# Kernel optimization log

Hardware: AMD Instinct MI355X
Metric: run time of the kernel (lower is better)

The kernel has to match this reference:

```python
import jax, jax.numpy as jnp
import numpy as np
from math import factorial

PI_A = 3.1415926  # the literal used in the original module
L = 16
NORDER = 5
PERIOD = 200.0


def _lpmv(m, n, x):
    """Associated Legendre P_n^m(x), m>=0, with Condon-Shortley phase (scipy convention)."""
    pmm = np.ones_like(x)
    if m > 0:
        dfact = float(np.prod(np.arange(1, 2 * m, 2, dtype=np.float64)))  # (2m-1)!!
        pmm = ((-1.0) ** m) * dfact * (1.0 - x * x) ** (m / 2.0)
    if n == m:
        return pmm
    pmmp1 = x * (2 * m + 1) * pmm
    if n == m + 1:
        return pmmp1
    for ll in range(m + 2, n + 1):
        pll = ((2 * ll - 1) * x * pmmp1 - (ll + m - 1) * pmm) / (ll - m)
        pmm, pmmp1 = pmmp1, pll
    return pmmp1


def _sh(m, n, ph, th):
    """Real SH matching the original `sh` helper. NOTE: the original uses `-1 ** m`,
    which in Python is -(1**m) == -1 for all m; we reproduce that faithfully."""
    ma = abs(m)
    N = np.sqrt((2 * n + 1) / (4.0 * np.pi) * factorial(n - ma) / factorial(n + ma))
    P = _lpmv(ma, n, np.cos(th))
    if m < 0:
        return (-np.sqrt(2.0) * N * P * np.sin(ma * ph)).astype(np.float32)
    if m == 0:
        return (N * P).astype(np.float32)
    return (-np.sqrt(2.0) * N * P * np.cos(ma * ph)).astype(np.float32)


def _grids():
    th, ph = np.meshgrid(
        (np.arange(L, dtype=np.float64) + 0.5) * PI_A / L,
        (np.arange(2 * L, dtype=np.float64) + 0.5) * PI_A / L,
        indexing='ij',
    )
    return th, ph  # each [L, 2L]


def setup_inputs() -> dict:
    key = jax.random.key(0)
    B = 65536
    lightid = jax.random.randint(key, (B,), 0, 256, dtype=jnp.int32)  # values unused; only size matters
    th, ph = _grids()
    mlist = [x for m in range(NORDER) for x in range(-m, m + 1)]
    nlist = [m for m in range(NORDER) for x in range(-m, m + 1)]
    bases = np.stack([_sh(m, n, ph, th) for m, n in zip(mlist, nlist)], axis=0)  # [25, L, 2L]
    return {"lightid": lightid, "iternum": 1000, "bases": jnp.asarray(bases)}


def reference(lightid, iternum, bases):
    B = lightid.shape[0]
    th_np, ph_np = _grids()
    th = jnp.asarray(th_np, dtype=jnp.float32)   # [L, 2L]
    ph = jnp.asarray(ph_np, dtype=jnp.float32)

    # Rotating light direction, computed in float64 (matches original per-sample python floats)
    ph0 = (iternum * B + np.arange(B, dtype=np.float64)) * 2.0 * PI_A / PERIOD  # [B]
    ldir = jnp.asarray(
        np.stack([np.sin(ph0), np.zeros(B), np.cos(ph0)], axis=-1).astype(np.float32)
    )  # [B, 3]

    # Per-pixel ray directions on the sphere grid
    dr = jnp.stack([jnp.sin(th) * jnp.sin(ph), jnp.cos(th), jnp.sin(th) * jnp.cos(ph)], axis=-1)  # [L, 2L, 3]

    dot = jnp.clip(jnp.einsum('bc,yxc->byx', ldir, dr), -1.0, 1.0)          # [B, L, 2L]
    lm = jnp.log(1e-5 + jnp.exp(-4.0 * jnp.arccos(dot) ** 2))               # gaussian lobe in log space
    lm = lm + 7.0 - jax.nn.logsumexp(lm, axis=(1, 2), keepdims=True)        # normalize total energy

    # SH projection: fold sin(theta) area weight and pi^2/numel into the basis
    numel = L * 2 * L
    w = bases * jnp.sin(th[:, 0])[None, :, None] * (np.pi ** 2 / numel)     # [25, L, 2L]
    proj = jnp.einsum('byx,kyx->bk', lm + 0.001, w)                         # [B, 25]

    return jnp.repeat(proj, 3, axis=1)
```

## Files before the change

### kernel.cpp

```cpp
#include <hip/hip_runtime.h>
#include <math.h>


#define PI_A 3.1415926
#define NPI  3.14159265358979323846

#if __has_builtin(__builtin_amdgcn_sqrtf)
#define FSQRT __builtin_amdgcn_sqrtf
#else
#define FSQRT sqrtf
#endif
#if __has_builtin(__builtin_amdgcn_exp2f)
#define FEXP2 __builtin_amdgcn_exp2f
#else
#define FEXP2 exp2f
#endif
#if __has_builtin(__builtin_amdgcn_logf)
#define FLOG2 __builtin_amdgcn_logf
#else
#define FLOG2 log2f
#endif

#define WT_OFF   0
#define WSUM_OFF 6400
#define TBL_OFF  6432

__global__ __launch_bounds__(256) void sh_prep_kernel(
        const float* __restrict__ bases, float* __restrict__ ws) {
    const int tid = threadIdx.x;
    const int k   = blockIdx.x;
    const float KC = (float)(NPI * NPI / 512.0);

    const int p = tid;
    const int y = p >> 5, x = p & 31;
    const float th_lo = (float)(((double)y + 0.5) * PI_A / 16.0);
    const float th_hi = (float)(((double)(15 - y) + 0.5) * PI_A / 16.0);
    const float v = bases[k * 512 + p] * (sinf(th_lo) * KC)
                  + bases[k * 512 + ((15 - y) << 5) + x] * (sinf(th_hi) * KC);
    ws[WT_OFF + p * 25 + k] = v;

    float s = v;
#pragma unroll
    for (int off = 32; off; off >>= 1) s += __shfl_down(s, off, 64);
    __shared__ float red[4];
    if ((tid & 63) == 0) red[tid >> 6] = s;
    __syncthreads();
    if (tid == 0) ws[WSUM_OFF + k] = red[0] + red[1] + red[2] + red[3];
}

__global__ __launch_bounds__(256) void sh_table_kernel(
        const int* __restrict__ iternum_p, float* __restrict__ ws, int B) {
    __shared__ float lmbuf[8 * 33];
    __shared__ float partial[8][26];
    __shared__ float Sred[4];

    const int tid = threadIdx.x;
    const int j   = blockIdx.x;

    const long long n = (long long)(*iternum_p) * (long long)B + (long long)j;
    const double ph0 = ((double)n * 2.0) * PI_A / 200.0;
    const float sld = (float)sin(ph0);
    const float cld = (float)cos(ph0);

    const int y = tid >> 5, x = tid & 31;
    const float th = (float)(((double)y + 0.5) * PI_A / 16.0);
    const float ph = (float)(((double)x + 0.5) * PI_A / 16.0);
    const float st  = sinf(th);
    const float drx = st * sinf(ph);
    const float drz = st * cosf(ph);
    float dot = fminf(1.0f, fmaxf(-1.0f, sld * drx + cld * drz));
    const float ax = fabsf(dot);
    const float sq = FSQRT(1.0f - ax);
    const float P  = fmaf(fmaf(fmaf(-0.0187293f, ax, 0.0742610f),
                               ax, -0.2121144f), ax, 1.5707288f);
    const float r_ = sq * P;
    const float a  = (dot < 0.0f) ? (3.14159265f - r_) : r_;
    const float c1 = -4.0f * 1.4426950408889634f;
    const float ln2 = 0.6931471805599453f;
    const float ex = FEXP2(a * a * c1);
    const float e  = 1e-5f + ex;
    const float lm = FLOG2(e) * ln2;
    lmbuf[(tid >> 5) * 33 + (tid & 31)] = lm;

    float s = e;
#pragma unroll
    for (int off = 32; off; off >>= 1) s += __shfl_down(s, off, 64);
    if ((tid & 63) == 0) Sred[tid >> 6] = s;
    __syncthreads();

    const int g = tid >> 5, k = tid & 31;
    if (k < 25) {
        float acc = 0.0f;
#pragma unroll
        for (int j2 = 0; j2 < 32; ++j2) {
            acc = fmaf(lmbuf[g * 33 + j2],
                       ws[WT_OFF + (g * 32 + j2) * 25 + k], acc);
        }
        partial[g][k] = acc;
    }
    __syncthreads();

    if (tid < 25) {
        float tot = 0.0f;
#pragma unroll
        for (int gg = 0; gg < 8; ++gg) tot += partial[gg][tid];
        const float S = Sred[0] + Sred[1] + Sred[2] + Sred[3];
        const float C = (7.0f - FLOG2(2.0f * S) * ln2) + 0.001f;
        const float v = tot + C * ws[WSUM_OFF + tid];
        float* tb = ws + TBL_OFF + j * 75 + 3 * tid;
        tb[0] = v; tb[1] = v; tb[2] = v;
    }
}

__global__ __launch_bounds__(256) void sh_bcast_kernel(
        const float* __restrict__ ws, float4* __restrict__ out, int total4) {
    const float4* t4 = (const float4*)(ws + TBL_OFF);
    int i = blockIdx.x * 256 + threadIdx.x;
    const int stride = gridDim.x * 256;
    for (; i < total4; i += stride)
        out[i] = t4[i % 3750];
}

extern "C" void kernel_launch(void* const* d_in, const int* in_sizes, int n_in,
                              void* d_out, int out_size, void* d_ws, size_t ws_size,
                              hipStream_t stream) {
    const int* iternum = (const int*)d_in[1];
    const float* bases = (const float*)d_in[2];
    float* ws = (float*)d_ws;
    const int B = in_sizes[0];
    const int total4 = out_size / 4;

    hipLaunchKernelGGL(sh_prep_kernel, dim3(25), dim3(256), 0, stream, bases, ws);
    hipLaunchKernelGGL(sh_table_kernel, dim3(200), dim3(256), 0, stream,
                       iternum, ws, B);
    int nblk = (total4 + 255) / 256;
    if (nblk > 2048) nblk = 2048;
    hipLaunchKernelGGL(sh_bcast_kernel, dim3(nblk), dim3(256), 0, stream,
                       ws, (float4*)d_out, total4);
}
```

Measured before the change: 18.07 us.

## Fuse prep, table and broadcast kernels into one single-launch kernel

```diff
diff --git a/kernel.cpp b/kernel.cpp
--- a/kernel.cpp
+++ b/kernel.cpp
@@ -4,6 +4,7 @@
 
 #define PI_A 3.1415926
 #define NPI  3.14159265358979323846
+#define SPLIT 4
 
 #if __has_builtin(__builtin_amdgcn_sqrtf)
 #define FSQRT __builtin_amdgcn_sqrtf
@@ -21,51 +22,40 @@
 #define FLOG2 log2f
 #endif
 
-#define WT_OFF   0
-#define WSUM_OFF 6400
-#define TBL_OFF  6432
+__global__ __launch_bounds__(256) void sh_fused_kernel(
+        const int* __restrict__ iternum_p, const float* __restrict__ bases,
+        float* __restrict__ out, int B) {
+    __shared__ float wt[256 * 25];
+    __shared__ float lmbuf[8 * 33];
+    __shared__ float partial[8][26];
+    __shared__ float wpartial[8][26];
+    __shared__ float Sred[4];
+    __shared__ float vrow[76];
 
-__global__ __launch_bounds__(256) void sh_prep_kernel(
-        const float* __restrict__ bases, float* __restrict__ ws) {
     const int tid = threadIdx.x;
-    const int k   = blockIdx.x;
-    const float KC = (float)(NPI * NPI / 512.0);
+    const int j   = blockIdx.x % 200;
+    const int s   = blockIdx.x / 200;
 
-    const int p = tid;
-    const int y = p >> 5, x = p & 31;
+    const float KC  = (float)(NPI * NPI / 512.0);
+    const float ln2 = 0.6931471805599453f;
+
+    const int p = tid, y = p >> 5, x = p & 31;
     const float th_lo = (float)(((double)y + 0.5) * PI_A / 16.0);
     const float th_hi = (float)(((double)(15 - y) + 0.5) * PI_A / 16.0);
-    const float v = bases[k * 512 + p] * (sinf(th_lo) * KC)
-                  + bases[k * 512 + ((15 - y) << 5) + x] * (sinf(th_hi) * KC);
-    ws[WT_OFF + p * 25 + k] = v;
-
-    float s = v;
+    const float st_lo = sinf(th_lo) * KC;
+    const float st_hi = sinf(th_hi) * KC;
+    const int mir = ((15 - y) << 5) + x;
 #pragma unroll
-    for (int off = 32; off; off >>= 1) s += __shfl_down(s, off, 64);
-    __shared__ float red[4];
-    if ((tid & 63) == 0) red[tid >> 6] = s;
-    __syncthreads();
-    if (tid == 0) ws[WSUM_OFF + k] = red[0] + red[1] + red[2] + red[3];
-}
-
-__global__ __launch_bounds__(256) void sh_table_kernel(
-        const int* __restrict__ iternum_p, float* __restrict__ ws, int B) {
-    __shared__ float lmbuf[8 * 33];
-    __shared__ float partial[8][26];
-    __shared__ float Sred[4];
-
-    const int tid = threadIdx.x;
-    const int j   = blockIdx.x;
+    for (int k = 0; k < 25; ++k)
+        wt[p * 25 + k] = bases[k * 512 + p] * st_lo + bases[k * 512 + mir] * st_hi;
 
     const long long n = (long long)(*iternum_p) * (long long)B + (long long)j;
     const double ph0 = ((double)n * 2.0) * PI_A / 200.0;
     const float sld = (float)sin(ph0);
     const float cld = (float)cos(ph0);
 
-    const int y = tid >> 5, x = tid & 31;
-    const float th = (float)(((double)y + 0.5) * PI_A / 16.0);
-    const float ph = (float)(((double)x + 0.5) * PI_A / 16.0);
-    const float st  = sinf(th);
+    const float ph  = (float)(((double)x + 0.5) * PI_A / 16.0);
+    const float st  = sinf(th_lo);
     const float drx = st * sinf(ph);
     const float drz = st * cosf(ph);
     float dot = fminf(1.0f, fmaxf(-1.0f, sld * drx + cld * drz));
@@ -76,49 +66,51 @@
     const float r_ = sq * P;
     const float a  = (dot < 0.0f) ? (3.14159265f - r_) : r_;
     const float c1 = -4.0f * 1.4426950408889634f;
-    const float ln2 = 0.6931471805599453f;
     const float ex = FEXP2(a * a * c1);
     const float e  = 1e-5f + ex;
     const float lm = FLOG2(e) * ln2;
-    lmbuf[(tid >> 5) * 33 + (tid & 31)] = lm;
+    lmbuf[y * 33 + x] = lm;
 
-    float s = e;
+    float sr = e;
 #pragma unroll
-    for (int off = 32; off; off >>= 1) s += __shfl_down(s, off, 64);
-    if ((tid & 63) == 0) Sred[tid >> 6] = s;
+    for (int off = 32; off; off >>= 1) sr += __shfl_down(sr, off, 64);
+    if ((tid & 63) == 0) Sred[tid >> 6] = sr;
     __syncthreads();
 
     const int g = tid >> 5, k = tid & 31;
     if (k < 25) {
-        float acc = 0.0f;
+        float acc = 0.0f, wacc = 0.0f;
 #pragma unroll
         for (int j2 = 0; j2 < 32; ++j2) {
-            acc = fmaf(lmbuf[g * 33 + j2],
-                       ws[WT_OFF + (g * 32 + j2) * 25 + k], acc);
+            const float w = wt[(g * 32 + j2) * 25 + k];
+            acc  = fmaf(lmbuf[g * 33 + j2], w, acc);
+            wacc += w;
         }
-        partial[g][k] = acc;
+        partial[g][k]  = acc;
+        wpartial[g][k] = wacc;
     }
     __syncthreads();
 
     if (tid < 25) {
-        float tot = 0.0f;
+        float tot = 0.0f, wsum = 0.0f;
 #pragma unroll
-        for (int gg = 0; gg < 8; ++gg) tot += partial[gg][tid];
+        for (int gg = 0; gg < 8; ++gg) { tot += partial[gg][tid]; wsum += wpartial[gg][tid]; }
         const float S = Sred[0] + Sred[1] + Sred[2] + Sred[3];
         const float C = (7.0f - FLOG2(2.0f * S) * ln2) + 0.001f;
-        const float v = tot + C * ws[WSUM_OFF + tid];
-        float* tb = ws + TBL_OFF + j * 75 + 3 * tid;
-        tb[0] = v; tb[1] = v; tb[2] = v;
+        const float v = tot + C * wsum;
+        vrow[3 * tid] = v; vrow[3 * tid + 1] = v; vrow[3 * tid + 2] = v;
     }
-}
+    __syncthreads();
 
-__global__ __launch_bounds__(256) void sh_bcast_kernel(
-        const float* __restrict__ ws, float4* __restrict__ out, int total4) {
-    const float4* t4 = (const float4*)(ws + TBL_OFF);
-    int i = blockIdx.x * 256 + threadIdx.x;
-    const int stride = gridDim.x * 256;
-    for (; i < total4; i += stride)
-        out[i] = t4[i % 3750];
+    const int b0 = j + 200 * s;
+    const int nrep = (B - b0 + 200 * SPLIT - 1) / (200 * SPLIT);
+    float* pb = out + (size_t)b0 * 75;
+    int rr = tid / 75, o = tid - rr * 75;
+    while (rr < nrep) {
+        pb[(size_t)rr * (200 * SPLIT * 75) + o] = vrow[o];
+        o += 31; rr += 3;
+        if (o >= 75) { o -= 75; rr += 1; }
+    }
 }
 
 extern "C" void kernel_launch(void* const* d_in, const int* in_sizes, int n_in,
@@ -126,15 +118,9 @@
                               hipStream_t stream) {
     const int* iternum = (const int*)d_in[1];
     const float* bases = (const float*)d_in[2];
-    float* ws = (float*)d_ws;
+    float* out = (float*)d_out;
     const int B = in_sizes[0];
-    const int total4 = out_size / 4;
 
-    hipLaunchKernelGGL(sh_prep_kernel, dim3(25), dim3(256), 0, stream, bases, ws);
-    hipLaunchKernelGGL(sh_table_kernel, dim3(200), dim3(256), 0, stream,
-                       iternum, ws, B);
-    int nblk = (total4 + 255) / 256;
-    if (nblk > 2048) nblk = 2048;
-    hipLaunchKernelGGL(sh_bcast_kernel, dim3(nblk), dim3(256), 0, stream,
-                       ws, (float4*)d_out, total4);
+    hipLaunchKernelGGL(sh_fused_kernel, dim3(200 * SPLIT), dim3(256), 0, stream,
+                       iternum, bases, out, B);
 }
```

New measurement: 14.88 us. 1.21x faster.
